# Kernel tuning notes

Hardware: AMD Instinct MI355X
Metric: run time of the kernel (lower is better)

## Reference

```python
import jax, jax.numpy as jnp
import numpy as np

# loss hyper-parameters (from settings.loss_settings defaults)
DICE_W, BOUNDARY_W, FOCAL_W = 1.0, 1.0, 1.0
FOCAL_ALPHA, FOCAL_GAMMA = 0.25, 2.0
EPS = 1e-6
INF = 1e10  # sentinel for 'no foreground pixel'


def _edt(fg):
    """Exact Euclidean distance transform to nearest True pixel.
    fg: [H, W] bool. Returns [H, W] float32 distances.
    Separable exact formulation: min_q (py-qy)^2 + (px-qx)^2
      = min_qy [ (py-qy)^2 + min_{qx: fg[qy,qx]} (px-qx)^2 ].
    Matches the brute-force all-pairs min of the torch code.
    """
    H, W = fg.shape
    ax = jnp.arange(W, dtype=jnp.float32)
    dx2 = (ax[:, None] - ax[None, :]) ** 2                      # [px, qx]
    # d1[qy, px] = min over qx in foreground row qy of (px-qx)^2
    d1 = jnp.where(fg[:, None, :], dx2[None, :, :], INF).min(-1)  # [qy, px]
    ay = jnp.arange(H, dtype=jnp.float32)
    dy2 = (ay[:, None] - ay[None, :]) ** 2                      # [py, qy]
    d = (dy2[:, :, None] + d1[None, :, :]).min(1)               # [py, px]
    # empty-foreground fallback: torch fills with sqrt((H-1)^2+(W-1)^2)
    max_d2 = float((H - 1) ** 2 + (W - 1) ** 2)
    d = jnp.where(d > INF * 0.5, max_d2, d)
    return jnp.sqrt(d)


def _signed_dist(gt):
    # gt: [1, H, W] float. phi_G = -dist_inside on fg, +dist_outside on bg.
    gb = gt[0] > 0.5
    dist_outside = _edt(gb)
    dist_inside = _edt(~gb)
    return jnp.where(gb, -dist_inside, dist_outside)[None]  # [1, H, W]


def setup_inputs() -> dict:
    key = jax.random.key(0)
    k1, k2 = jax.random.split(key)
    pred_masks = jax.random.normal(k1, (8, 1, 256, 256), dtype=jnp.float32)
    target_masks = jax.random.uniform(k2, (8, 1, 256, 256), dtype=jnp.float32)
    return {"pred_masks": pred_masks, "target_masks": target_masks}


def reference(pred_masks, target_masks):
    t = target_masks.astype(jnp.float32)
    p = jax.nn.sigmoid(pred_masks)

    # dice loss
    inter = (p * t).sum(axis=(2, 3))
    union = p.sum(axis=(2, 3)) + t.sum(axis=(2, 3))
    dice_val = 1.0 - ((2.0 * inter + EPS) / (union + EPS)).mean()

    # boundary loss: signed distance map of gt (sequential over batch to cap memory)
    phi_G = jax.lax.map(_signed_dist, t)  # [N, 1, H, W]
    boundary_val = (phi_G * p).mean()

    # focal loss
    pc = jnp.clip(p, EPS, 1.0 - EPS)
    pt = pc * t + (1.0 - pc) * (1.0 - t)
    alpha_t = FOCAL_ALPHA * t + (1.0 - FOCAL_ALPHA) * (1.0 - t)
    focal_val = (-alpha_t * (1.0 - pt) ** FOCAL_GAMMA * jnp.log(pt)).mean()

    loss = DICE_W * dice_val + BOUNDARY_W * boundary_val + FOCAL_W * focal_val
    return (loss, dice_val, boundary_val, focal_val)
```

## Files before the change

kernel.cpp:

```cpp
#include <hip/hip_runtime.h>
#include <math.h>
#include <limits.h>

constexpr int N = 8;
constexpr int H = 256;
constexpr int W = 256;
constexpr int NPIX = N * H * W;
constexpr float FEPS = 1e-6f;
constexpr int   RSENT = 20000;
constexpr int   EMPTY_THRESH = 300000000;
constexpr int   NROW = N * H;
constexpr int   NBLK = NROW / 2;
constexpr int   BIGC = 1 << 20;
constexpr unsigned long long MAGIC = 0x9E3779B97F4A7C15ull;


__device__ __forceinline__ void wave_scan_row(const float4 tv, const int lane,
                                              int rf[4], int rb[4])
{
    const int px0 = lane << 2;
    const float tvv[4] = {tv.x, tv.y, tv.z, tv.w};
    int af[4], ab[4], bf[4], bb[4];
    #pragma unroll
    for (int k = 0; k < 4; ++k) {
        const bool fg = tvv[k] > 0.5f;
        const int cf = fg ? 0 : BIGC;
        const int cb = fg ? BIGC : 0;
        af[k] = cf - (px0 + k);
        ab[k] = cb - (px0 + k);
        bf[k] = cf + (px0 + k);
        bb[k] = cb + (px0 + k);
    }
    int pf[4], pb[4], qf[4], qb[4];
    pf[0] = af[0]; pb[0] = ab[0];
    #pragma unroll
    for (int k = 1; k < 4; ++k) { pf[k] = min(pf[k-1], af[k]); pb[k] = min(pb[k-1], ab[k]); }
    qf[3] = bf[3]; qb[3] = bb[3];
    #pragma unroll
    for (int k = 2; k >= 0; --k) { qf[k] = min(qf[k+1], bf[k]); qb[k] = min(qb[k+1], bb[k]); }

    int sf = pf[3], sb = pb[3], tf = qf[0], tb = qb[0];
    #pragma unroll
    for (int off = 1; off < 64; off <<= 1) {
        const int uf = __shfl_up(sf, off, 64);
        const int ub = __shfl_up(sb, off, 64);
        const int df = __shfl_down(tf, off, 64);
        const int db = __shfl_down(tb, off, 64);
        if (lane >= off)      { sf = min(sf, uf); sb = min(sb, ub); }
        if (lane + off < 64)  { tf = min(tf, df); tb = min(tb, db); }
    }
    int ef = __shfl_up(sf, 1, 64);   if (lane == 0)  ef = INT_MAX / 2;
    int eb = __shfl_up(sb, 1, 64);   if (lane == 0)  eb = INT_MAX / 2;
    int xf = __shfl_down(tf, 1, 64); if (lane == 63) xf = INT_MAX / 2;
    int xb = __shfl_down(tb, 1, 64); if (lane == 63) xb = INT_MAX / 2;

    #pragma unroll
    for (int k = 0; k < 4; ++k) {
        const int p = px0 + k;
        int F  = p + min(ef, pf[k]);
        int Bv = min(xf, qf[k]) - p;
        int r  = min(F, Bv); if (r > 255) r = RSENT;
        rf[k] = r;
        F  = p + min(eb, pb[k]);
        Bv = min(xb, qb[k]) - p;
        r  = min(F, Bv); if (r > 255) r = RSENT;
        rb[k] = r;
    }
}

__global__ __launch_bounds__(256, 2) void fused_kernel(
    const float* __restrict__ pred, const float* __restrict__ tgt,
    float* __restrict__ parts, unsigned long long* __restrict__ flags,
    float* __restrict__ out)
{
    const int blk  = blockIdx.x;
    const int n    = blk >> 7;
    const int py0  = (blk & 127) << 1;
    const int py1  = py0 + 1;
    const int px   = threadIdx.x;
    const int lane = px & 63;
    const int wid  = px >> 6;

    __shared__ unsigned int rows[8][W];
    __shared__ float smem[2][20];
    __shared__ float smf[8];
    __shared__ float sratio[8];

    const float* __restrict__ timg = tgt  + (size_t)n * (H * W);
    const float* __restrict__ pimg = pred + (size_t)n * (H * W);

    {
        const int s1 = wid, s2 = wid + 4;
        const int qy1 = py0 - 3 + s1;
        const int qy2 = py0 - 3 + s2;
        const bool va = (qy1 >= 0) & (qy1 < H);
        const bool vb = (qy2 >= 0) & (qy2 < H);
        float4 tva, tvb;
        if (va) tva = *(const float4*)(timg + qy1 * W + (lane << 2));
        if (vb) tvb = *(const float4*)(timg + qy2 * W + (lane << 2));
        if (va) {
            int rf[4], rb[4];
            wave_scan_row(tva, lane, rf, rb);
            uint4 pk;
            pk.x = (unsigned)rf[0] | ((unsigned)rb[0] << 16);
            pk.y = (unsigned)rf[1] | ((unsigned)rb[1] << 16);
            pk.z = (unsigned)rf[2] | ((unsigned)rb[2] << 16);
            pk.w = (unsigned)rf[3] | ((unsigned)rb[3] << 16);
            *(uint4*)&rows[s1][lane << 2] = pk;
        }
        if (vb) {
            int rf[4], rb[4];
            wave_scan_row(tvb, lane, rf, rb);
            uint4 pk;
            pk.x = (unsigned)rf[0] | ((unsigned)rb[0] << 16);
            pk.y = (unsigned)rf[1] | ((unsigned)rb[1] << 16);
            pk.z = (unsigned)rf[2] | ((unsigned)rb[2] << 16);
            pk.w = (unsigned)rf[3] | ((unsigned)rb[3] << 16);
            *(uint4*)&rows[s2][lane << 2] = pk;
        }
    }

    const float x0 = pimg[py0 * W + px];
    const float x1 = pimg[py1 * W + px];
    const float t0 = timg[py0 * W + px];
    const float t1 = timg[py1 * W + px];

    __syncthreads();

    int bf0 = INT_MAX, bb0 = INT_MAX, bf1 = INT_MAX, bb1 = INT_MAX;
    #pragma unroll
    for (int s = 0; s < 8; ++s) {
        const int qy = py0 - 3 + s;
        if (qy >= 0 && qy < H) {
            const unsigned v = rows[s][px];
            const int rfv = (int)(v & 0xffffu);
            const int rbv = (int)(v >> 16);
            const int rf2 = rfv * rfv, rb2 = rbv * rbv;
            const int d0 = s - 3, d1 = s - 4;
            bf0 = min(bf0, rf2 + d0 * d0); bb0 = min(bb0, rb2 + d0 * d0);
            bf1 = min(bf1, rf2 + d1 * d1); bb1 = min(bb1, rb2 + d1 * d1);
        }
    }

    for (int qy = py0 - 4; qy >= 0; --qy) {
        const int du0 = py0 - qy, du1 = du0 + 1;
        const int d0s = du0 * du0, d1s = du1 * du1;
        if (!__any((d0s < bf0) | (d0s < bb0) | (d1s < bf1) | (d1s < bb1))) break;
        const float4 tv = *(const float4*)(timg + qy * W + (lane << 2));
        int rf[4], rb[4];
        wave_scan_row(tv, lane, rf, rb);
        const int o = px >> 2;
        const int k = px & 3;
        int f0 = __shfl(rf[0], o, 64), f1 = __shfl(rf[1], o, 64);
        int f2 = __shfl(rf[2], o, 64), f3 = __shfl(rf[3], o, 64);
        int g0 = __shfl(rb[0], o, 64), g1 = __shfl(rb[1], o, 64);
        int g2 = __shfl(rb[2], o, 64), g3 = __shfl(rb[3], o, 64);
        const int irf = (k == 0) ? f0 : (k == 1) ? f1 : (k == 2) ? f2 : f3;
        const int irb = (k == 0) ? g0 : (k == 1) ? g1 : (k == 2) ? g2 : g3;
        const int rf2 = irf * irf, rb2 = irb * irb;
        bf0 = min(bf0, rf2 + d0s); bb0 = min(bb0, rb2 + d0s);
        bf1 = min(bf1, rf2 + d1s); bb1 = min(bb1, rb2 + d1s);
    }
    for (int qy = py0 + 5; qy < H; ++qy) {
        const int dd0 = qy - py0, dd1 = dd0 - 1;
        const int d0s = dd0 * dd0, d1s = dd1 * dd1;
        if (!__any((d0s < bf0) | (d0s < bb0) | (d1s < bf1) | (d1s < bb1))) break;
        const float4 tv = *(const float4*)(timg + qy * W + (lane << 2));
        int rf[4], rb[4];
        wave_scan_row(tv, lane, rf, rb);
        const int o = px >> 2;
        const int k = px & 3;
        int f0 = __shfl(rf[0], o, 64), f1 = __shfl(rf[1], o, 64);
        int f2 = __shfl(rf[2], o, 64), f3 = __shfl(rf[3], o, 64);
        int g0 = __shfl(rb[0], o, 64), g1 = __shfl(rb[1], o, 64);
        int g2 = __shfl(rb[2], o, 64), g3 = __shfl(rb[3], o, 64);
        const int irf = (k == 0) ? f0 : (k == 1) ? f1 : (k == 2) ? f2 : f3;
        const int irb = (k == 0) ? g0 : (k == 1) ? g1 : (k == 2) ? g2 : g3;
        const int rf2 = irf * irf, rb2 = irb * irb;
        bf0 = min(bf0, rf2 + d0s); bb0 = min(bb0, rb2 + d0s);
        bf1 = min(bf1, rf2 + d1s); bb1 = min(bb1, rb2 + d1s);
    }

    const float MAXD2 = (float)((H - 1) * (H - 1) + (W - 1) * (W - 1));
    const float Df0 = (bf0 > EMPTY_THRESH) ? MAXD2 : (float)bf0;
    const float Db0 = (bb0 > EMPTY_THRESH) ? MAXD2 : (float)bb0;
    const float Df1 = (bf1 > EMPTY_THRESH) ? MAXD2 : (float)bf1;
    const float Db1 = (bb1 > EMPTY_THRESH) ? MAXD2 : (float)bb1;

    const float p0   = 1.0f / (1.0f + expf(-x0));
    const float phi0 = (t0 > 0.5f) ? -sqrtf(Db0) : sqrtf(Df0);
    const float pc0  = fminf(fmaxf(p0, FEPS), 1.0f - FEPS);
    const float pt0  = pc0 * t0 + (1.0f - pc0) * (1.0f - t0);
    const float at0  = 0.25f * t0 + 0.75f * (1.0f - t0);
    const float om0  = 1.0f - pt0;
    const float fo0  = -at0 * om0 * om0 * logf(pt0);

    const float p1   = 1.0f / (1.0f + expf(-x1));
    const float phi1 = (t1 > 0.5f) ? -sqrtf(Db1) : sqrtf(Df1);
    const float pc1  = fminf(fmaxf(p1, FEPS), 1.0f - FEPS);
    const float pt1  = pc1 * t1 + (1.0f - pc1) * (1.0f - t1);
    const float at1  = 0.25f * t1 + 0.75f * (1.0f - t1);
    const float om1  = 1.0f - pt1;
    const float fo1  = -at1 * om1 * om1 * logf(pt1);

    float v50[5] = { p0 * t0, p0, t0, phi0 * p0, fo0 };
    float v51[5] = { p1 * t1, p1, t1, phi1 * p1, fo1 };
    #pragma unroll
    for (int q = 0; q < 5; ++q) {
        float a = v50[q], b = v51[q];
        #pragma unroll
        for (int off = 32; off > 0; off >>= 1) {
            a += __shfl_down(a, off, 64);
            b += __shfl_down(b, off, 64);
        }
        v50[q] = a; v51[q] = b;
    }
    if (lane == 0) {
        #pragma unroll
        for (int q = 0; q < 5; ++q) {
            smem[0][wid * 5 + q] = v50[q];
            smem[1][wid * 5 + q] = v51[q];
        }
    }
    __syncthreads();
    if (px == 0) {
        #pragma unroll
        for (int r = 0; r < 2; ++r) {
            #pragma unroll
            for (int q = 0; q < 5; ++q) {
                const float v = smem[r][q] + smem[r][5 + q] + smem[r][10 + q] + smem[r][15 + q];
                __hip_atomic_store(&parts[q * NROW + blk * 2 + r], v,
                                   __ATOMIC_RELAXED, __HIP_MEMORY_SCOPE_AGENT);
            }
        }
        asm volatile("s_waitcnt vmcnt(0)" ::: "memory");
        __hip_atomic_store(&flags[blk], MAGIC, __ATOMIC_RELAXED, __HIP_MEMORY_SCOPE_AGENT);
    }

    if (blk == 0) {
        const int tid = px;
        bool done = false;
        int guard = 0;
        do {
            bool mine = true;
            #pragma unroll
            for (int k = 0; k < NBLK / 256; ++k) {
                const unsigned long long v = __hip_atomic_load(
                    &flags[tid + k * 256], __ATOMIC_RELAXED, __HIP_MEMORY_SCOPE_AGENT);
                mine = mine && (v == MAGIC);
            }
            done = (__syncthreads_and((int)mine) != 0);
            if (!done) __builtin_amdgcn_s_sleep(2);
        } while (!done && (++guard < (1 << 26)));

        float bp = 0.0f, fc = 0.0f;
        for (int k = tid; k < NROW; k += 256) {
            bp += __hip_atomic_load(&parts[3 * NROW + k], __ATOMIC_RELAXED, __HIP_MEMORY_SCOPE_AGENT);
            fc += __hip_atomic_load(&parts[4 * NROW + k], __ATOMIC_RELAXED, __HIP_MEMORY_SCOPE_AGENT);
        }
        #pragma unroll
        for (int off = 32; off > 0; off >>= 1) {
            bp += __shfl_down(bp, off, 64);
            fc += __shfl_down(fc, off, 64);
        }
        if (lane == 0) { smf[wid * 2] = bp; smf[wid * 2 + 1] = fc; }

        #pragma unroll
        for (int mi = 0; mi < 2; ++mi) {
            const int m = wid * 2 + mi;
            float A = 0.f, S = 0.f, C = 0.f;
            #pragma unroll
            for (int k = 0; k < 4; ++k) {
                const int i = m * 256 + k * 64 + lane;
                A += __hip_atomic_load(&parts[0 * NROW + i], __ATOMIC_RELAXED, __HIP_MEMORY_SCOPE_AGENT);
                S += __hip_atomic_load(&parts[1 * NROW + i], __ATOMIC_RELAXED, __HIP_MEMORY_SCOPE_AGENT);
                C += __hip_atomic_load(&parts[2 * NROW + i], __ATOMIC_RELAXED, __HIP_MEMORY_SCOPE_AGENT);
            }
            #pragma unroll
            for (int off = 32; off > 0; off >>= 1) {
                A += __shfl_down(A, off, 64);
                S += __shfl_down(S, off, 64);
                C += __shfl_down(C, off, 64);
            }
            if (lane == 0) sratio[m] = (2.0f * A + FEPS) / (S + C + FEPS);
        }
        __syncthreads();
        if (tid == 0) {
            const float B = smf[0] + smf[2] + smf[4] + smf[6];
            const float F = smf[1] + smf[3] + smf[5] + smf[7];
            float dacc = 0.0f;
            #pragma unroll
            for (int m = 0; m < 8; ++m) dacc += sratio[m];
            const float dice_val     = 1.0f - dacc / (float)N;
            const float boundary_val = B / (float)NPIX;
            const float focal_val    = F / (float)NPIX;
            out[0] = dice_val + boundary_val + focal_val;
            out[1] = dice_val;
            out[2] = boundary_val;
            out[3] = focal_val;
        }
    }
}

extern "C" void kernel_launch(void* const* d_in, const int* in_sizes, int n_in,
                              void* d_out, int out_size, void* d_ws, size_t ws_size,
                              hipStream_t stream)
{
    const float* pred = (const float*)d_in[0];
    const float* tgt  = (const float*)d_in[1];
    float* out = (float*)d_out;

    float* parts = (float*)d_ws;
    unsigned long long* flags =
        (unsigned long long*)((char*)d_ws + (size_t)5 * NROW * sizeof(float));

    fused_kernel<<<NBLK, 256, 0, stream>>>(pred, tgt, parts, flags, out);
}
```

Measured before the change: 70.16 us.

## Replace shuffle-based row min-scans with ballot bitmasks and ffs/clz distance lookup

The per-row 1D nearest-foreground and nearest-background distance computation moves off a 6-step shuffle prefix/suffix min-scan. Each row is now turned into four 64-bit ballot masks, and each lane finds its nearest set bit left and right with ffs/clz, carrying over across the 64-bit words. The far-row loops now compute only the lane's own pixel value, so the per-row shuffle redistribution goes away. Launch bounds are raised to 4 blocks per CU to allow more occupancy, which risks register pressure.

After: 67.73 us, median of 2. 3.5% less time.

```diff
diff --git a/kernel.cpp b/kernel.cpp
--- a/kernel.cpp
+++ b/kernel.cpp
@@ -11,64 +11,42 @@
 constexpr int   EMPTY_THRESH = 300000000;
 constexpr int   NROW = N * H;
 constexpr int   NBLK = NROW / 2;
-constexpr int   BIGC = 1 << 20;
+constexpr int   BIGD = 1 << 20;
 constexpr unsigned long long MAGIC = 0x9E3779B97F4A7C15ull;
 
 
-__device__ __forceinline__ void wave_scan_row(const float4 tv, const int lane,
-                                              int rf[4], int rb[4])
+__device__ __forceinline__ void mask_dists(
+    const unsigned long long m0, const unsigned long long m1,
+    const unsigned long long m2, const unsigned long long m3,
+    const int lane, int r[4])
 {
-    const int px0 = lane << 2;
-    const float tvv[4] = {tv.x, tv.y, tv.z, tv.w};
-    int af[4], ab[4], bf[4], bb[4];
+    const int f1 = __ffsll((long long)m1), f2 = __ffsll((long long)m2), f3 = __ffsll((long long)m3);
+    const int d3 = f3 ? f3 - 1 : BIGD;
+    const int d2 = f2 ? f2 - 1 : 64 + d3;
+    const int d1 = f1 ? f1 - 1 : 64 + d2;
+    const int c0 = __clzll((long long)m0), c1 = __clzll((long long)m1), c2 = __clzll((long long)m2);
+    const int e0 = (c0 < 64) ? c0 : BIGD;
+    const int e1 = (c1 < 64) ? c1 : 64 + e0;
+    const int e2 = (c2 < 64) ? c2 : 64 + e1;
+
+    const unsigned long long mw[4] = {m0, m1, m2, m3};
+    const int dnx[4] = {d1, d2, d3, BIGD};
+    const int epv[4] = {BIGD, e0, e1, e2};
     #pragma unroll
     for (int k = 0; k < 4; ++k) {
-        const bool fg = tvv[k] > 0.5f;
-        const int cf = fg ? 0 : BIGC;
-        const int cb = fg ? BIGC : 0;
-        af[k] = cf - (px0 + k);
-        ab[k] = cb - (px0 + k);
-        bf[k] = cf + (px0 + k);
-        bb[k] = cb + (px0 + k);
-    }
-    int pf[4], pb[4], qf[4], qb[4];
-    pf[0] = af[0]; pb[0] = ab[0];
-    #pragma unroll
-    for (int k = 1; k < 4; ++k) { pf[k] = min(pf[k-1], af[k]); pb[k] = min(pb[k-1], ab[k]); }
-    qf[3] = bf[3]; qb[3] = bb[3];
-    #pragma unroll
-    for (int k = 2; k >= 0; --k) { qf[k] = min(qf[k+1], bf[k]); qb[k] = min(qb[k+1], bb[k]); }
-
-    int sf = pf[3], sb = pb[3], tf = qf[0], tb = qb[0];
-    #pragma unroll
-    for (int off = 1; off < 64; off <<= 1) {
-        const int uf = __shfl_up(sf, off, 64);
-        const int ub = __shfl_up(sb, off, 64);
-        const int df = __shfl_down(tf, off, 64);
-        const int db = __shfl_down(tb, off, 64);
-        if (lane >= off)      { sf = min(sf, uf); sb = min(sb, ub); }
-        if (lane + off < 64)  { tf = min(tf, df); tb = min(tb, db); }
-    }
-    int ef = __shfl_up(sf, 1, 64);   if (lane == 0)  ef = INT_MAX / 2;
-    int eb = __shfl_up(sb, 1, 64);   if (lane == 0)  eb = INT_MAX / 2;
-    int xf = __shfl_down(tf, 1, 64); if (lane == 63) xf = INT_MAX / 2;
-    int xb = __shfl_down(tb, 1, 64); if (lane == 63) xb = INT_MAX / 2;
-
-    #pragma unroll
-    for (int k = 0; k < 4; ++k) {
-        const int p = px0 + k;
-        int F  = p + min(ef, pf[k]);
-        int Bv = min(xf, qf[k]) - p;
-        int r  = min(F, Bv); if (r > 255) r = RSENT;
-        rf[k] = r;
-        F  = p + min(eb, pb[k]);
-        Bv = min(xb, qb[k]) - p;
-        r  = min(F, Bv); if (r > 255) r = RSENT;
-        rb[k] = r;
+        const unsigned long long x = mw[k] >> lane;
+        const int fx = __ffsll((long long)x);
+        const int dR = fx ? fx - 1 : (64 - lane) + dnx[k];
+        const unsigned long long y = mw[k] << (63 - lane);
+        const int cy = __clzll((long long)y);
+        const int dL = (cy < 64) ? cy : (lane + 1) + epv[k];
+        int rr = min(dL, dR);
+        if (rr > 255) rr = RSENT;
+        r[k] = rr;
     }
 }
 
-__global__ __launch_bounds__(256, 2) void fused_kernel(
+__global__ __launch_bounds__(256, 4) void fused_kernel(
     const float* __restrict__ pred, const float* __restrict__ tgt,
     float* __restrict__ parts, unsigned long long* __restrict__ flags,
     float* __restrict__ out)
@@ -89,34 +67,25 @@
     const float* __restrict__ timg = tgt  + (size_t)n * (H * W);
     const float* __restrict__ pimg = pred + (size_t)n * (H * W);
 
-    {
-        const int s1 = wid, s2 = wid + 4;
-        const int qy1 = py0 - 3 + s1;
-        const int qy2 = py0 - 3 + s2;
-        const bool va = (qy1 >= 0) & (qy1 < H);
-        const bool vb = (qy2 >= 0) & (qy2 < H);
-        float4 tva, tvb;
-        if (va) tva = *(const float4*)(timg + qy1 * W + (lane << 2));
-        if (vb) tvb = *(const float4*)(timg + qy2 * W + (lane << 2));
-        if (va) {
+    #pragma unroll
+    for (int sh = 0; sh < 2; ++sh) {
+        const int s  = wid + sh * 4;
+        const int qy = py0 - 3 + s;
+        if (qy >= 0 && qy < H) {
+            const float a0 = timg[qy * W + lane];
+            const float a1 = timg[qy * W + 64 + lane];
+            const float a2 = timg[qy * W + 128 + lane];
+            const float a3 = timg[qy * W + 192 + lane];
+            const unsigned long long m0 = __ballot(a0 > 0.5f);
+            const unsigned long long m1 = __ballot(a1 > 0.5f);
+            const unsigned long long m2 = __ballot(a2 > 0.5f);
+            const unsigned long long m3 = __ballot(a3 > 0.5f);
             int rf[4], rb[4];
-            wave_scan_row(tva, lane, rf, rb);
-            uint4 pk;
-            pk.x = (unsigned)rf[0] | ((unsigned)rb[0] << 16);
-            pk.y = (unsigned)rf[1] | ((unsigned)rb[1] << 16);
-            pk.z = (unsigned)rf[2] | ((unsigned)rb[2] << 16);
-            pk.w = (unsigned)rf[3] | ((unsigned)rb[3] << 16);
-            *(uint4*)&rows[s1][lane << 2] = pk;
-        }
-        if (vb) {
-            int rf[4], rb[4];
-            wave_scan_row(tvb, lane, rf, rb);
-            uint4 pk;
-            pk.x = (unsigned)rf[0] | ((unsigned)rb[0] << 16);
-            pk.y = (unsigned)rf[1] | ((unsigned)rb[1] << 16);
-            pk.z = (unsigned)rf[2] | ((unsigned)rb[2] << 16);
-            pk.w = (unsigned)rf[3] | ((unsigned)rb[3] << 16);
-            *(uint4*)&rows[s2][lane << 2] = pk;
+            mask_dists(m0, m1, m2, m3, lane, rf);
+            mask_dists(~m0, ~m1, ~m2, ~m3, lane, rb);
+            #pragma unroll
+            for (int k = 0; k < 4; ++k)
+                rows[s][(k << 6) + lane] = (unsigned)rf[k] | ((unsigned)rb[k] << 16);
         }
     }
 
@@ -136,49 +105,76 @@
             const int rfv = (int)(v & 0xffffu);
             const int rbv = (int)(v >> 16);
             const int rf2 = rfv * rfv, rb2 = rbv * rbv;
-            const int d0 = s - 3, d1 = s - 4;
-            bf0 = min(bf0, rf2 + d0 * d0); bb0 = min(bb0, rb2 + d0 * d0);
-            bf1 = min(bf1, rf2 + d1 * d1); bb1 = min(bb1, rb2 + d1 * d1);
-        }
-    }
-
-    for (int qy = py0 - 4; qy >= 0; --qy) {
-        const int du0 = py0 - qy, du1 = du0 + 1;
-        const int d0s = du0 * du0, d1s = du1 * du1;
-        if (!__any((d0s < bf0) | (d0s < bb0) | (d1s < bf1) | (d1s < bb1))) break;
-        const float4 tv = *(const float4*)(timg + qy * W + (lane << 2));
-        int rf[4], rb[4];
-        wave_scan_row(tv, lane, rf, rb);
-        const int o = px >> 2;
-        const int k = px & 3;
-        int f0 = __shfl(rf[0], o, 64), f1 = __shfl(rf[1], o, 64);
-        int f2 = __shfl(rf[2], o, 64), f3 = __shfl(rf[3], o, 64);
-        int g0 = __shfl(rb[0], o, 64), g1 = __shfl(rb[1], o, 64);
-        int g2 = __shfl(rb[2], o, 64), g3 = __shfl(rb[3], o, 64);
-        const int irf = (k == 0) ? f0 : (k == 1) ? f1 : (k == 2) ? f2 : f3;
-        const int irb = (k == 0) ? g0 : (k == 1) ? g1 : (k == 2) ? g2 : g3;
-        const int rf2 = irf * irf, rb2 = irb * irb;
-        bf0 = min(bf0, rf2 + d0s); bb0 = min(bb0, rb2 + d0s);
-        bf1 = min(bf1, rf2 + d1s); bb1 = min(bb1, rb2 + d1s);
-    }
-    for (int qy = py0 + 5; qy < H; ++qy) {
-        const int dd0 = qy - py0, dd1 = dd0 - 1;
-        const int d0s = dd0 * dd0, d1s = dd1 * dd1;
-        if (!__any((d0s < bf0) | (d0s < bb0) | (d1s < bf1) | (d1s < bb1))) break;
-        const float4 tv = *(const float4*)(timg + qy * W + (lane << 2));
-        int rf[4], rb[4];
-        wave_scan_row(tv, lane, rf, rb);
-        const int o = px >> 2;
-        const int k = px & 3;
-        int f0 = __shfl(rf[0], o, 64), f1 = __shfl(rf[1], o, 64);
-        int f2 = __shfl(rf[2], o, 64), f3 = __shfl(rf[3], o, 64);
-        int g0 = __shfl(rb[0], o, 64), g1 = __shfl(rb[1], o, 64);
-        int g2 = __shfl(rb[2], o, 64), g3 = __shfl(rb[3], o, 64);
-        const int irf = (k == 0) ? f0 : (k == 1) ? f1 : (k == 2) ? f2 : f3;
-        const int irb = (k == 0) ? g0 : (k == 1) ? g1 : (k == 2) ? g2 : g3;
-        const int rf2 = irf * irf, rb2 = irb * irb;
-        bf0 = min(bf0, rf2 + d0s); bb0 = min(bb0, rb2 + d0s);
-        bf1 = min(bf1, rf2 + d1s); bb1 = min(bb1, rb2 + d1s);
+            const int d0 = s - 3, d1v = s - 4;
+            bf0 = min(bf0, rf2 + d0 * d0);  bb0 = min(bb0, rb2 + d0 * d0);
+            bf1 = min(bf1, rf2 + d1v * d1v); bb1 = min(bb1, rb2 + d1v * d1v);
+        }
+    }
+
+    for (int dir = 0; dir < 2; ++dir) {
+        const int qy_start = dir ? py0 + 5 : py0 - 4;
+        const int qy_step  = dir ? 1 : -1;
+        for (int qy = qy_start; qy >= 0 && qy < H; qy += qy_step) {
+            const int dd = dir ? (qy - py0) : (py0 - qy);
+            const int du1 = dir ? (dd - 1) : (dd + 1);
+            const int d0s = dd * dd, d1s = du1 * du1;
+            if (!__any((d0s < bf0) | (d0s < bb0) | (d1s < bf1) | (d1s < bb1))) break;
+            const float a0 = timg[qy * W + lane];
+            const float a1 = timg[qy * W + 64 + lane];
+            const float a2 = timg[qy * W + 128 + lane];
+            const float a3 = timg[qy * W + 192 + lane];
+            const unsigned long long m0 = __ballot(a0 > 0.5f);
+            const unsigned long long m1 = __ballot(a1 > 0.5f);
+            const unsigned long long m2 = __ballot(a2 > 0.5f);
+            const unsigned long long m3 = __ballot(a3 > 0.5f);
+            int rfv, rbv;
+            {
+                const int f1 = __ffsll((long long)m1), f2 = __ffsll((long long)m2), f3 = __ffsll((long long)m3);
+                const int d3 = f3 ? f3 - 1 : BIGD;
+                const int d2 = f2 ? f2 - 1 : 64 + d3;
+                const int d1c = f1 ? f1 - 1 : 64 + d2;
+                const int c0 = __clzll((long long)m0), c1 = __clzll((long long)m1), c2 = __clzll((long long)m2);
+                const int e0 = (c0 < 64) ? c0 : BIGD;
+                const int e1 = (c1 < 64) ? c1 : 64 + e0;
+                const int e2 = (c2 < 64) ? c2 : 64 + e1;
+                const unsigned long long mw = (wid == 0) ? m0 : (wid == 1) ? m1 : (wid == 2) ? m2 : m3;
+                const int dnx = (wid == 0) ? d1c : (wid == 1) ? d2 : (wid == 2) ? d3 : BIGD;
+                const int epv = (wid == 0) ? BIGD : (wid == 1) ? e0 : (wid == 2) ? e1 : e2;
+                const unsigned long long x = mw >> lane;
+                const int fx = __ffsll((long long)x);
+                const int dR = fx ? fx - 1 : (64 - lane) + dnx;
+                const unsigned long long y = mw << (63 - lane);
+                const int cy = __clzll((long long)y);
+                const int dL = (cy < 64) ? cy : (lane + 1) + epv;
+                int rr = min(dL, dR); if (rr > 255) rr = RSENT;
+                rfv = rr;
+            }
+            {
+                const unsigned long long b0 = ~m0, b1 = ~m1, b2 = ~m2, b3 = ~m3;
+                const int f1 = __ffsll((long long)b1), f2 = __ffsll((long long)b2), f3 = __ffsll((long long)b3);
+                const int d3 = f3 ? f3 - 1 : BIGD;
+                const int d2 = f2 ? f2 - 1 : 64 + d3;
+                const int d1c = f1 ? f1 - 1 : 64 + d2;
+                const int c0 = __clzll((long long)b0), c1 = __clzll((long long)b1), c2 = __clzll((long long)b2);
+                const int e0 = (c0 < 64) ? c0 : BIGD;
+                const int e1 = (c1 < 64) ? c1 : 64 + e0;
+                const int e2 = (c2 < 64) ? c2 : 64 + e1;
+                const unsigned long long mw = (wid == 0) ? b0 : (wid == 1) ? b1 : (wid == 2) ? b2 : b3;
+                const int dnx = (wid == 0) ? d1c : (wid == 1) ? d2 : (wid == 2) ? d3 : BIGD;
+                const int epv = (wid == 0) ? BIGD : (wid == 1) ? e0 : (wid == 2) ? e1 : e2;
+                const unsigned long long x = mw >> lane;
+                const int fx = __ffsll((long long)x);
+                const int dR = fx ? fx - 1 : (64 - lane) + dnx;
+                const unsigned long long y = mw << (63 - lane);
+                const int cy = __clzll((long long)y);
+                const int dL = (cy < 64) ? cy : (lane + 1) + epv;
+                int rr = min(dL, dR); if (rr > 255) rr = RSENT;
+                rbv = rr;
+            }
+            const int rf2 = rfv * rfv, rb2 = rbv * rbv;
+            bf0 = min(bf0, rf2 + d0s); bb0 = min(bb0, rb2 + d0s);
+            bf1 = min(bf1, rf2 + d1s); bb1 = min(bb1, rb2 + d1s);
+        }
     }
 
     const float MAXD2 = (float)((H - 1) * (H - 1) + (W - 1) * (W - 1));
```
